# Performance work log

Hardware: AMD Instinct MI355X
Metric: run time of the kernel (lower is better)

## Reference

```python
import jax, jax.numpy as jnp
import numpy as np


def setup_inputs() -> dict:
    key = jax.random.key(0)
    ks = jax.random.split(key, 8)
    N, DIN, DOUT = 8192, 1024, 1024
    s = 1.0 / np.sqrt(DIN)
    return {
        "gAB": jax.random.normal(ks[0], (N, DIN), dtype=jnp.float32),
        "gAG": jax.random.normal(ks[1], (N, DIN), dtype=jnp.float32),
        "Wab": jax.random.normal(ks[2], (DIN, DOUT), dtype=jnp.float32) * s,
        "Wag": jax.random.normal(ks[3], (DIN, DOUT), dtype=jnp.float32) * s,
        "bab": jax.random.normal(ks[4], (DOUT,), dtype=jnp.float32) * 0.01,
        "bag": jax.random.normal(ks[5], (DOUT,), dtype=jnp.float32) * 0.01,
        "sAB": jax.random.normal(ks[6], (N, DOUT), dtype=jnp.float32),
        "sAG": jax.random.normal(ks[7], (N, DOUT), dtype=jnp.float32),
    }


def reference(gAB, gAG, Wab, Wag, bab, bag, sAB, sAG) -> jnp.ndarray:
    # project() per encoder (Linear): [N, DIN] @ [DIN, DOUT] + b
    pAB = gAB @ Wab + bab  # [N, DOUT]
    pAG = gAG @ Wag + bag  # [N, DOUT]
    # torch.diag(pAB @ pAG.T) == row-wise dot product (avoids O(N^2 d) waste)
    h1 = jnp.sum(pAB * pAG, axis=1, keepdims=True)  # [N, 1]
    h2 = jnp.sum(sAB * sAG, axis=1, keepdims=True)  # [N, 1]
    # mean over concatenated (h1, h2) columns, keepdim=True
    h = jnp.mean(jnp.concatenate([h1, h2], axis=1), axis=1, keepdims=True)  # [N, 1]
    return h
```

## Files before the change

### kernel.cpp

```cpp
#include <hip/hip_runtime.h>
#include <hip/hip_bf16.h>
#include <stdint.h>

typedef __attribute__((ext_vector_type(8))) short bf16x8;
typedef __attribute__((ext_vector_type(4))) float f32x4;

#define DIN 1024
#define NROWS 8192

__device__ __forceinline__ unsigned short f2bf(float f) {
    union { float f; unsigned u; } v; v.f = f;
    unsigned r = v.u + 0x7FFFu + ((v.u >> 16) & 1u);
    return (unsigned short)(r >> 16);
}

__device__ __forceinline__ int fswz(int r) { return (r ^ (r >> 2)) & 3; }

__device__ __forceinline__ size_t swz_byte(int R, int col) {
    return ((size_t)R * DIN + (col & ~31)) * 2 + (size_t)((((col >> 3) & 3) ^ fswz(R)) << 4) + (size_t)((col & 7) * 2);
}

__device__ __forceinline__ void gload_lds16(const void* g, void* l) {
    __builtin_amdgcn_global_load_lds(
        (const __attribute__((address_space(1))) unsigned*)g,
        (__attribute__((address_space(3))) unsigned*)l, 16, 0, 0);
}

__global__ __launch_bounds__(256) void prep_kernel(const float* __restrict__ Wab,
                                                   const float* __restrict__ Wag,
                                                   const float* __restrict__ bab,
                                                   const float* __restrict__ bag,
                                                   float* __restrict__ ws_f,
                                                   unsigned short* __restrict__ Whab,
                                                   unsigned short* __restrict__ Whag) {
    int b = blockIdx.x;
    int wave = threadIdx.x >> 6, lane = threadIdx.x & 63;
    if (b == 256) {
        if (wave == 0) {
            float acc = 0.f;
            for (int j = lane; j < DIN; j += 64) acc += bab[j] * bag[j];
            for (int off = 32; off; off >>= 1) acc += __shfl_xor(acc, off);
            if (lane == 0) ws_f[2048] = acc;
        }
        return;
    }
    int r = b * 4 + wave;
    int fr = fswz(r);
    {
        const float* wrow = Wab + (size_t)r * DIN;
        char* hrow = (char*)Whab + (size_t)r * DIN * 2;
        float acc = 0.f;
#pragma unroll
        for (int it = 0; it < 4; ++it) {
            int col = it * 256 + lane * 4;
            float4 w = *reinterpret_cast<const float4*>(wrow + col);
            float4 bv = *reinterpret_cast<const float4*>(bag + col);
            acc += w.x * bv.x + w.y * bv.y + w.z * bv.z + w.w * bv.w;
            ushort4 h; h.x = f2bf(w.x); h.y = f2bf(w.y); h.z = f2bf(w.z); h.w = f2bf(w.w);
            *reinterpret_cast<ushort4*>(hrow + (col & ~31) * 2 + ((((col >> 3) & 3) ^ fr) << 4) + (col & 7) * 2) = h;
        }
        for (int off = 32; off; off >>= 1) acc += __shfl_xor(acc, off);
        if (lane == 0) ws_f[r] = acc;
    }
    {
        const float* wrow = Wag + (size_t)r * DIN;
        char* hrow = (char*)Whag + (size_t)r * DIN * 2;
        float acc = 0.f;
#pragma unroll
        for (int it = 0; it < 4; ++it) {
            int col = it * 256 + lane * 4;
            float4 w = *reinterpret_cast<const float4*>(wrow + col);
            float4 bv = *reinterpret_cast<const float4*>(bab + col);
            acc += w.x * bv.x + w.y * bv.y + w.z * bv.z + w.w * bv.w;
            ushort4 h; h.x = f2bf(w.x); h.y = f2bf(w.y); h.z = f2bf(w.z); h.w = f2bf(w.w);
            *reinterpret_cast<ushort4*>(hrow + (col & ~31) * 2 + ((((col >> 3) & 3) ^ fr) << 4) + (col & 7) * 2) = h;
        }
        for (int off = 32; off; off >>= 1) acc += __shfl_xor(acc, off);
        if (lane == 0) ws_f[1024 + r] = acc;
    }
}

__global__ __launch_bounds__(512) void mt_kernel(const unsigned short* __restrict__ Whag,
                                                 const unsigned short* __restrict__ Whab,
                                                 unsigned short* __restrict__ Mt) {
    __shared__ unsigned short sm[2][2][2][2048];
    int tid = threadIdx.x;
    int wave = tid >> 6, grp = wave >> 2, w4 = wave & 3;
    int lane = tid & 63, kg = lane >> 4, cl = lane & 15;
    int wr = w4 >> 1, wc = w4 & 1;
    int br = blockIdx.x >> 4, bc = blockIdx.x & 15;
    int u = tid & 255, urow = u >> 2, uchunk = u & 3;

    const char* Abase = (const char*)Whag + ((size_t)(br * 64 + urow) * DIN + grp * 512) * 2 + uchunk * 16;
    const char* Bbase = (const char*)Whab + ((size_t)(bc * 64 + urow) * DIN + grp * 512) * 2 + uchunk * 16;

    int offA[2], offB[2];
#pragma unroll
    for (int m = 0; m < 2; ++m) { int row = wr * 32 + m * 16 + cl; offA[m] = row * 32 + ((kg ^ fswz(row)) << 3); }
#pragma unroll
    for (int n = 0; n < 2; ++n) { int row = wc * 32 + n * 16 + cl; offB[n] = row * 32 + ((kg ^ fswz(row)) << 3); }

    f32x4 acc[2][2] = {};
    gload_lds16(Abase, &sm[grp][0][0][u * 8]);
    gload_lds16(Bbase, &sm[grp][0][1][u * 8]);
    for (int t = 0; t < 16; ++t) {
        int p = t & 1;
        __syncthreads();
        if (t < 15) {
            gload_lds16(Abase + (t + 1) * 64, &sm[grp][p ^ 1][0][u * 8]);
            gload_lds16(Bbase + (t + 1) * 64, &sm[grp][p ^ 1][1][u * 8]);
        }
        bf16x8 af[2], bfr[2];
#pragma unroll
        for (int m = 0; m < 2; ++m) af[m] = *reinterpret_cast<const bf16x8*>(&sm[grp][p][0][offA[m]]);
#pragma unroll
        for (int n = 0; n < 2; ++n) bfr[n] = *reinterpret_cast<const bf16x8*>(&sm[grp][p][1][offB[n]]);
        __builtin_amdgcn_s_setprio(1);
#pragma unroll
        for (int m = 0; m < 2; ++m)
#pragma unroll
            for (int n = 0; n < 2; ++n)
                acc[m][n] = __builtin_amdgcn_mfma_f32_16x16x32_bf16(af[m], bfr[n], acc[m][n], 0, 0, 0);
        __builtin_amdgcn_s_setprio(0);
    }
    __syncthreads();
    float* red = (float*)sm;
    if (grp == 1) {
#pragma unroll
        for (int m = 0; m < 2; ++m)
#pragma unroll
            for (int n = 0; n < 2; ++n)
#pragma unroll
                for (int j = 0; j < 4; ++j)
                    red[(wr * 32 + m * 16 + kg * 4 + j) * 68 + wc * 32 + n * 16 + cl] = acc[m][n][j];
    }
    __syncthreads();
    if (grp == 0) {
#pragma unroll
        for (int m = 0; m < 2; ++m)
#pragma unroll
            for (int n = 0; n < 2; ++n)
#pragma unroll
                for (int j = 0; j < 4; ++j) {
                    int rl = wr * 32 + m * 16 + kg * 4 + j, cll = wc * 32 + n * 16 + cl;
                    float v = acc[m][n][j] + red[rl * 68 + cll];
                    int R = br * 64 + rl, C = bc * 64 + cll;
                    *(unsigned short*)((char*)Mt + swz_byte(R, C & ~3) + (C & 3) * 2) = f2bf(v);
                }
    }
}

__global__ __launch_bounds__(256) void stream_kernel(const float* __restrict__ gAB,
                                                     const float* __restrict__ sAB,
                                                     const float* __restrict__ sAG,
                                                     const float* __restrict__ ws_f,
                                                     unsigned short* __restrict__ gABh,
                                                     float* __restrict__ out,
                                                     int writecast) {
    int wave = threadIdx.x >> 6, lane = threadIdx.x & 63;
    int row = blockIdx.x * 4 + wave;
    const float* ga = gAB + (size_t)row * DIN;
    const float* sa = sAB + (size_t)row * DIN;
    const float* sg = sAG + (size_t)row * DIN;
    char* gh = (char*)gABh + (size_t)row * DIN * 2;
    int fr = fswz(row);
    float acc = 0.f;
#pragma unroll
    for (int cc = 0; cc < 4; ++cc) {
        int col = cc * 256 + lane * 4;
        float4 a = *reinterpret_cast<const float4*>(ga + col);
        float4 x = *reinterpret_cast<const float4*>(sa + col);
        float4 y = *reinterpret_cast<const float4*>(sg + col);
        float4 v = *reinterpret_cast<const float4*>(ws_f + col);
        acc += x.x * y.x + x.y * y.y + x.z * y.z + x.w * y.w;
        acc += a.x * v.x + a.y * v.y + a.z * v.z + a.w * v.w;
        if (writecast) {
            ushort4 h; h.x = f2bf(a.x); h.y = f2bf(a.y); h.z = f2bf(a.z); h.w = f2bf(a.w);
            *reinterpret_cast<ushort4*>(gh + (col & ~31) * 2 + ((((col >> 3) & 3) ^ fr) << 4) + (col & 7) * 2) = h;
        }
    }
#pragma unroll
    for (int off = 32; off; off >>= 1) acc += __shfl_xor(acc, off);
    if (lane == 0) out[row] = 0.5f * (acc + ws_f[2048]);
}

template <int PRECAST, int KSPLIT>
__global__ __launch_bounds__(256, 4) void gemm_kernel(const float* __restrict__ gAB,
                                                      const unsigned short* __restrict__ gABh,
                                                      const float* __restrict__ gAG,
                                                      const unsigned short* __restrict__ Mt,
                                                      const float* __restrict__ ws_f,
                                                      float* __restrict__ out) {
    __shared__ unsigned short lds_a[2][128 * 32];
    __shared__ unsigned short lds_b[2][128 * 32];
    constexpr int KLEN = DIN / KSPLIT;
    constexpr int NSTEP = KLEN / 32;
    int b = blockIdx.x;
    int x = b & 7, s = b >> 3;
    int rblk = x + 8 * (s & 7);
    int u2 = s >> 3;
    int ks = u2 & (KSPLIT - 1);
    int cblk = u2 / KSPLIT;
    int tid = threadIdx.x, wave = tid >> 6, lane = tid & 63;
    int wr = wave >> 1, wc = wave & 1;
    int kg = lane >> 4, cl = lane & 15;
    int row0 = rblk * 128, col0 = cblk * 128;

    int offA[4], offB[4];
#pragma unroll
    for (int m = 0; m < 4; ++m) { int row = wr * 64 + m * 16 + cl; offA[m] = row * 32 + ((kg ^ fswz(row)) << 3); }
#pragma unroll
    for (int n = 0; n < 4; ++n) { int row = wc * 64 + n * 16 + cl; offB[n] = row * 32 + ((kg ^ fswz(row)) << 3); }

    size_t kofs = (size_t)(ks * KLEN) * 2;
    const char* Ab = (const char*)gABh + (size_t)row0 * DIN * 2 + kofs;
    const char* Bb = (const char*)Mt + (size_t)col0 * DIN * 2 + kofs;
    int u0 = tid, u1 = tid + 256;
    size_t a0 = (size_t)(u0 >> 2) * (DIN * 2) + (u0 & 3) * 16;
    size_t a1 = (size_t)(u1 >> 2) * (DIN * 2) + (u1 & 3) * 16;

    f32x4 acc[4][4] = {};
    float4 ra[4];
    if (PRECAST) {
        gload_lds16(Ab + a0, (char*)&lds_a[0][0] + u0 * 16);
        gload_lds16(Ab + a1, (char*)&lds_a[0][0] + u1 * 16);
        gload_lds16(Bb + a0, (char*)&lds_b[0][0] + u0 * 16);
        gload_lds16(Bb + a1, (char*)&lds_b[0][0] + u1 * 16);

        for (int t = 0; t < NSTEP; ++t) {
            int p = t & 1;
            __syncthreads();
            if (t < NSTEP - 1) {
                gload_lds16(Ab + a0 + (t + 1) * 64, (char*)&lds_a[p ^ 1][0] + u0 * 16);
                gload_lds16(Ab + a1 + (t + 1) * 64, (char*)&lds_a[p ^ 1][0] + u1 * 16);
                gload_lds16(Bb + a0 + (t + 1) * 64, (char*)&lds_b[p ^ 1][0] + u0 * 16);
                gload_lds16(Bb + a1 + (t + 1) * 64, (char*)&lds_b[p ^ 1][0] + u1 * 16);
            }
            bf16x8 af[4], bfr[4];
#pragma unroll
            for (int m = 0; m < 4; ++m) af[m] = *reinterpret_cast<const bf16x8*>(&lds_a[p][offA[m]]);
#pragma unroll
            for (int n = 0; n < 4; ++n) bfr[n] = *reinterpret_cast<const bf16x8*>(&lds_b[p][offB[n]]);
            __builtin_amdgcn_s_setprio(1);
#pragma unroll
            for (int m = 0; m < 4; ++m)
#pragma unroll
                for (int n = 0; n < 4; ++n)
                    acc[m][n] = __builtin_amdgcn_mfma_f32_16x16x32_bf16(af[m], bfr[n], acc[m][n], 0, 0, 0);
            __builtin_amdgcn_s_setprio(0);
        }
    } else {
#pragma unroll
        for (int it = 0; it < 4; ++it) {
            int u = tid + it * 256;
            ra[it] = *reinterpret_cast<const float4*>(gAB + (size_t)(row0 + (u >> 3)) * DIN + ks * KLEN + (u & 7) * 4);
        }
#pragma unroll
        for (int it = 0; it < 4; ++it) {
            int u = tid + it * 256, row = u >> 3, c4 = u & 7;
            ushort4 h; h.x = f2bf(ra[it].x); h.y = f2bf(ra[it].y); h.z = f2bf(ra[it].z); h.w = f2bf(ra[it].w);
            *reinterpret_cast<ushort4*>((char*)&lds_a[0][0] + row * 64 + ((((c4 >> 1) ^ fswz(row))) << 4) + (c4 & 1) * 8) = h;
        }
        gload_lds16(Bb + a0, (char*)&lds_b[0][0] + u0 * 16);
        gload_lds16(Bb + a1, (char*)&lds_b[0][0] + u1 * 16);
        for (int t = 0; t < NSTEP; ++t) {
            int p = t & 1;
            __syncthreads();
            if (t < NSTEP - 1) {
#pragma unroll
                for (int it = 0; it < 4; ++it) {
                    int u = tid + it * 256;
                    ra[it] = *reinterpret_cast<const float4*>(gAB + (size_t)(row0 + (u >> 3)) * DIN + ks * KLEN + (t + 1) * 32 + (u & 7) * 4);
                }
                gload_lds16(Bb + a0 + (t + 1) * 64, (char*)&lds_b[p ^ 1][0] + u0 * 16);
                gload_lds16(Bb + a1 + (t + 1) * 64, (char*)&lds_b[p ^ 1][0] + u1 * 16);
            }
            bf16x8 af[4], bfr[4];
#pragma unroll
            for (int m = 0; m < 4; ++m) af[m] = *reinterpret_cast<const bf16x8*>(&lds_a[p][offA[m]]);
#pragma unroll
            for (int n = 0; n < 4; ++n) bfr[n] = *reinterpret_cast<const bf16x8*>(&lds_b[p][offB[n]]);
#pragma unroll
            for (int m = 0; m < 4; ++m)
#pragma unroll
                for (int n = 0; n < 4; ++n)
                    acc[m][n] = __builtin_amdgcn_mfma_f32_16x16x32_bf16(af[m], bfr[n], acc[m][n], 0, 0, 0);
            if (t < NSTEP - 1) {
#pragma unroll
                for (int it = 0; it < 4; ++it) {
                    int u = tid + it * 256, row = u >> 3, c4 = u & 7;
                    ushort4 h; h.x = f2bf(ra[it].x); h.y = f2bf(ra[it].y); h.z = f2bf(ra[it].z); h.w = f2bf(ra[it].w);
                    *reinterpret_cast<ushort4*>((char*)&lds_a[p ^ 1][0] + row * 64 + ((((c4 >> 1) ^ fswz(row))) << 4) + (c4 & 1) * 8) = h;
                }
            }
        }
    }

    const float* vag = ws_f + 1024;
#pragma unroll
    for (int m = 0; m < 4; ++m)
#pragma unroll
        for (int j = 0; j < 4; ++j) {
            int row = row0 + wr * 64 + m * 16 + kg * 4 + j;
            const float* gr = gAG + (size_t)row * DIN;
            float t = 0.f;
#pragma unroll
            for (int n = 0; n < 4; ++n) {
                int col = col0 + wc * 64 + n * 16 + cl;
                float addv = (ks == 0) ? vag[col] : 0.f;
                t += gr[col] * (acc[m][n][j] + addv);
            }
            t += __shfl_xor(t, 1);
            t += __shfl_xor(t, 2);
            t += __shfl_xor(t, 4);
            t += __shfl_xor(t, 8);
            if (cl == 0) atomicAdd(out + row, 0.5f * t);
        }
}

extern "C" void kernel_launch(void* const* d_in, const int* in_sizes, int n_in,
                              void* d_out, int out_size, void* d_ws, size_t ws_size,
                              hipStream_t stream) {
    const float* gAB = (const float*)d_in[0];
    const float* gAG = (const float*)d_in[1];
    const float* Wab = (const float*)d_in[2];
    const float* Wag = (const float*)d_in[3];
    const float* bab = (const float*)d_in[4];
    const float* bag = (const float*)d_in[5];
    const float* sAB = (const float*)d_in[6];
    const float* sAG = (const float*)d_in[7];
    float* out = (float*)d_out;

    float* ws_f = (float*)d_ws;
    char* base = (char*)d_ws + 16384;
    unsigned short* Mt = (unsigned short*)base;
    unsigned short* Whag = (unsigned short*)(base + (size_t)2 * 1024 * 1024);
    unsigned short* Whab = (unsigned short*)(base + (size_t)4 * 1024 * 1024);
    unsigned short* gABh = (unsigned short*)(base + (size_t)6 * 1024 * 1024);
    size_t need_full = 16384 + (size_t)22 * 1024 * 1024;
    int precast = (ws_size >= need_full) ? 1 : 0;

    prep_kernel<<<257, 256, 0, stream>>>(Wab, Wag, bab, bag, ws_f, Whab, Whag);
    mt_kernel<<<256, 512, 0, stream>>>(Whag, Whab, Mt);
    stream_kernel<<<2048, 256, 0, stream>>>(gAB, sAB, sAG, ws_f, gABh, out, precast);
    if (precast)
        gemm_kernel<1, 2><<<1024, 256, 0, stream>>>(gAB, gABh, gAG, Mt, ws_f, out);
    else
        gemm_kernel<0, 2><<<1024, 256, 0, stream>>>(gAB, gABh, gAG, Mt, ws_f, out);
}
```

Before: 67.15 us.

## Merge Mt GEMM and row-streaming kernels into one launch

Combines the independent Mt weight-product kernel and the row-streaming dot/cast kernel into a single grid: the first 256 blocks compute Mt with 256 threads each (wider per-wave N tile), and the remaining blocks do the streaming rows. This removes a launch boundary and lets the small GEMM overlap with the memory-bound streaming work. In exchange the Mt blocks use fewer threads and more accumulators, and both paths now share one register and LDS budget.

```diff
diff --git a/kernel.cpp b/kernel.cpp
--- a/kernel.cpp
+++ b/kernel.cpp
@@ -16,8 +16,10 @@
 
 __device__ __forceinline__ int fswz(int r) { return (r ^ (r >> 2)) & 3; }
 
-__device__ __forceinline__ size_t swz_byte(int R, int col) {
-    return ((size_t)R * DIN + (col & ~31)) * 2 + (size_t)((((col >> 3) & 3) ^ fswz(R)) << 4) + (size_t)((col & 7) * 2);
+__device__ __forceinline__ size_t swz_byte(int R, int c) {
+    return ((size_t)R * DIN + (size_t)(c & ~31)) * 2
+         + (size_t)((((c >> 3) & 3) ^ fswz(R)) << 4)
+         + (size_t)((c & 7) * 2);
 }
 
 __device__ __forceinline__ void gload_lds16(const void* g, void* l) {
@@ -80,85 +82,93 @@
     }
 }
 
-__global__ __launch_bounds__(512) void mt_kernel(const unsigned short* __restrict__ Whag,
-                                                 const unsigned short* __restrict__ Whab,
-                                                 unsigned short* __restrict__ Mt) {
+__global__ __launch_bounds__(256) void combo_kernel(const unsigned short* __restrict__ Whag,
+                                                    const unsigned short* __restrict__ Whab,
+                                                    unsigned short* __restrict__ Mt,
+                                                    const float* __restrict__ gAB,
+                                                    const float* __restrict__ sAB,
+                                                    const float* __restrict__ sAG,
+                                                    const float* __restrict__ ws_f,
+                                                    unsigned short* __restrict__ gABh,
+                                                    float* __restrict__ out,
+                                                    int writecast) {
     __shared__ unsigned short sm[2][2][2][2048];
-    int tid = threadIdx.x;
-    int wave = tid >> 6, grp = wave >> 2, w4 = wave & 3;
-    int lane = tid & 63, kg = lane >> 4, cl = lane & 15;
-    int wr = w4 >> 1, wc = w4 & 1;
-    int br = blockIdx.x >> 4, bc = blockIdx.x & 15;
-    int u = tid & 255, urow = u >> 2, uchunk = u & 3;
-
-    const char* Abase = (const char*)Whag + ((size_t)(br * 64 + urow) * DIN + grp * 512) * 2 + uchunk * 16;
-    const char* Bbase = (const char*)Whab + ((size_t)(bc * 64 + urow) * DIN + grp * 512) * 2 + uchunk * 16;
-
-    int offA[2], offB[2];
-#pragma unroll
-    for (int m = 0; m < 2; ++m) { int row = wr * 32 + m * 16 + cl; offA[m] = row * 32 + ((kg ^ fswz(row)) << 3); }
-#pragma unroll
-    for (int n = 0; n < 2; ++n) { int row = wc * 32 + n * 16 + cl; offB[n] = row * 32 + ((kg ^ fswz(row)) << 3); }
-
-    f32x4 acc[2][2] = {};
-    gload_lds16(Abase, &sm[grp][0][0][u * 8]);
-    gload_lds16(Bbase, &sm[grp][0][1][u * 8]);
-    for (int t = 0; t < 16; ++t) {
-        int p = t & 1;
+    int b = blockIdx.x;
+    int tid = threadIdx.x, wave = tid >> 6, lane = tid & 63;
+
+    if (b < 256) {
+        int grp = wave >> 1, w2 = wave & 1;
+        int kg = lane >> 4, cl = lane & 15;
+        int br = b >> 4, bc = b & 15;
+        int u = tid & 127;
+
+        const char* Abase = (const char*)Whag + ((size_t)(br * 64) * DIN + grp * 512) * 2;
+        const char* Bbase = (const char*)Whab + ((size_t)(bc * 64) * DIN + grp * 512) * 2;
+
+        int offA[2], offB[4];
+#pragma unroll
+        for (int m = 0; m < 2; ++m) { int row = w2 * 32 + m * 16 + cl; offA[m] = row * 32 + ((kg ^ fswz(row)) << 3); }
+#pragma unroll
+        for (int n = 0; n < 4; ++n) { int row = n * 16 + cl; offB[n] = row * 32 + ((kg ^ fswz(row)) << 3); }
+
+        f32x4 acc[2][4] = {};
+#define STAGE_MT(buf, t)                                                            \
+        _Pragma("unroll")                                                           \
+        for (int it = 0; it < 2; ++it) {                                            \
+            int un = u + it * 128, urow = un >> 2, uc = un & 3;                     \
+            gload_lds16(Abase + (size_t)urow * 2048 + (t) * 64 + uc * 16,           \
+                        &sm[grp][buf][0][un * 8]);                                  \
+            gload_lds16(Bbase + (size_t)urow * 2048 + (t) * 64 + uc * 16,           \
+                        &sm[grp][buf][1][un * 8]);                                  \
+        }
+        STAGE_MT(0, 0);
+        for (int t = 0; t < 16; ++t) {
+            int p = t & 1;
+            __syncthreads();
+            if (t < 15) { STAGE_MT(p ^ 1, t + 1); }
+            bf16x8 af[2], bfr[4];
+#pragma unroll
+            for (int m = 0; m < 2; ++m) af[m] = *reinterpret_cast<const bf16x8*>(&sm[grp][p][0][offA[m]]);
+#pragma unroll
+            for (int n = 0; n < 4; ++n) bfr[n] = *reinterpret_cast<const bf16x8*>(&sm[grp][p][1][offB[n]]);
+            __builtin_amdgcn_s_setprio(1);
+#pragma unroll
+            for (int m = 0; m < 2; ++m)
+#pragma unroll
+                for (int n = 0; n < 4; ++n)
+                    acc[m][n] = __builtin_amdgcn_mfma_f32_16x16x32_bf16(af[m], bfr[n], acc[m][n], 0, 0, 0);
+            __builtin_amdgcn_s_setprio(0);
+        }
+#undef STAGE_MT
         __syncthreads();
-        if (t < 15) {
-            gload_lds16(Abase + (t + 1) * 64, &sm[grp][p ^ 1][0][u * 8]);
-            gload_lds16(Bbase + (t + 1) * 64, &sm[grp][p ^ 1][1][u * 8]);
-        }
-        bf16x8 af[2], bfr[2];
-#pragma unroll
-        for (int m = 0; m < 2; ++m) af[m] = *reinterpret_cast<const bf16x8*>(&sm[grp][p][0][offA[m]]);
-#pragma unroll
-        for (int n = 0; n < 2; ++n) bfr[n] = *reinterpret_cast<const bf16x8*>(&sm[grp][p][1][offB[n]]);
-        __builtin_amdgcn_s_setprio(1);
-#pragma unroll
-        for (int m = 0; m < 2; ++m)
-#pragma unroll
-            for (int n = 0; n < 2; ++n)
-                acc[m][n] = __builtin_amdgcn_mfma_f32_16x16x32_bf16(af[m], bfr[n], acc[m][n], 0, 0, 0);
-        __builtin_amdgcn_s_setprio(0);
-    }
-    __syncthreads();
-    float* red = (float*)sm;
-    if (grp == 1) {
-#pragma unroll
-        for (int m = 0; m < 2; ++m)
-#pragma unroll
-            for (int n = 0; n < 2; ++n)
-#pragma unroll
-                for (int j = 0; j < 4; ++j)
-                    red[(wr * 32 + m * 16 + kg * 4 + j) * 68 + wc * 32 + n * 16 + cl] = acc[m][n][j];
-    }
-    __syncthreads();
-    if (grp == 0) {
-#pragma unroll
-        for (int m = 0; m < 2; ++m)
-#pragma unroll
-            for (int n = 0; n < 2; ++n)
-#pragma unroll
-                for (int j = 0; j < 4; ++j) {
-                    int rl = wr * 32 + m * 16 + kg * 4 + j, cll = wc * 32 + n * 16 + cl;
-                    float v = acc[m][n][j] + red[rl * 68 + cll];
-                    int R = br * 64 + rl, C = bc * 64 + cll;
-                    *(unsigned short*)((char*)Mt + swz_byte(R, C & ~3) + (C & 3) * 2) = f2bf(v);
-                }
-    }
-}
-
-__global__ __launch_bounds__(256) void stream_kernel(const float* __restrict__ gAB,
-                                                     const float* __restrict__ sAB,
-                                                     const float* __restrict__ sAG,
-                                                     const float* __restrict__ ws_f,
-                                                     unsigned short* __restrict__ gABh,
-                                                     float* __restrict__ out,
-                                                     int writecast) {
-    int wave = threadIdx.x >> 6, lane = threadIdx.x & 63;
-    int row = blockIdx.x * 4 + wave;
+        float* red = (float*)sm;
+        if (grp == 1) {
+#pragma unroll
+            for (int m = 0; m < 2; ++m)
+#pragma unroll
+                for (int n = 0; n < 4; ++n)
+#pragma unroll
+                    for (int j = 0; j < 4; ++j)
+                        red[(w2 * 32 + m * 16 + kg * 4 + j) * 68 + n * 16 + cl] = acc[m][n][j];
+        }
+        __syncthreads();
+        if (grp == 0) {
+#pragma unroll
+            for (int m = 0; m < 2; ++m)
+#pragma unroll
+                for (int n = 0; n < 4; ++n)
+#pragma unroll
+                    for (int j = 0; j < 4; ++j) {
+                        int rl = w2 * 32 + m * 16 + kg * 4 + j, cll = n * 16 + cl;
+                        float v = acc[m][n][j] + red[rl * 68 + cll];
+                        int R = br * 64 + rl, C = bc * 64 + cll;
+                        *(unsigned short*)((char*)Mt + swz_byte(R, C)) = f2bf(v);
+                    }
+        }
+        return;
+    }
+
+    int row = (b - 256) * 4 + wave;
     const float* ga = gAB + (size_t)row * DIN;
     const float* sa = sAB + (size_t)row * DIN;
     const float* sg = sAG + (size_t)row * DIN;
@@ -341,8 +351,7 @@
     int precast = (ws_size >= need_full) ? 1 : 0;
 
     prep_kernel<<<257, 256, 0, stream>>>(Wab, Wag, bab, bag, ws_f, Whab, Whag);
-    mt_kernel<<<256, 512, 0, stream>>>(Whag, Whab, Mt);
-    stream_kernel<<<2048, 256, 0, stream>>>(gAB, sAB, sAG, ws_f, gABh, out, precast);
+    combo_kernel<<<2304, 256, 0, stream>>>(Whag, Whab, Mt, gAB, sAB, sAG, ws_f, gABh, out, precast);
     if (precast)
         gemm_kernel<1, 2><<<1024, 256, 0, stream>>>(gAB, gABh, gAG, Mt, ws_f, out);
     else
```

Result: faster. 61.46 us (median of 2 runs) (-8.5%).
